# Optimization experiments

Measured on AMD Instinct MI355X. Metric: run time of the kernel, lower is better.

Reference implementation:

```python
import jax, jax.numpy as jnp
import numpy as np

EMB = 64
NUM_LAYERS = 2


def _mlp_embed(x, shift, scale, w1, b1, w2, b2):
    # PreNormLayer: (x + shift) * scale, then Linear-ReLU-Linear-ReLU
    x = (x + shift) * scale
    x = jax.nn.relu(x @ w1 + b1)
    return jax.nn.relu(x @ w2 + b2)


def _sage_conv(x_src, x_dst, src_idx, dst_idx, ll_w, ll_b, lr_w):
    # PyG SAGEConv: mean-aggregate gathered source features at destinations,
    # out = lin_l(mean) + lin_r(x_dst); lin_l has bias, lin_r does not.
    n_dst = x_dst.shape[0]
    msgs = x_src[src_idx]                                   # [E, D] gather
    ssum = jax.ops.segment_sum(msgs, dst_idx, num_segments=n_dst)
    cnt = jax.ops.segment_sum(jnp.ones(src_idx.shape[0], x_src.dtype),
                              dst_idx, num_segments=n_dst)
    mean = ssum / jnp.maximum(cnt, 1.0)[:, None]            # [n_dst, D]
    return mean @ ll_w + ll_b + x_dst @ lr_w


def setup_inputs() -> dict:
    key = jax.random.key(0)
    ks = jax.random.split(key, 20)
    n_cons, n_var, n_edges = 100_000, 200_000, 2_000_000
    cons_nf, var_nf, edge_nf = 5, 19, 1

    def lin(k, fan_in, fan_out):
        return jax.random.normal(k, (fan_in, fan_out), jnp.float32) / np.sqrt(fan_in)

    inp = {
        'cons_x': jax.random.normal(ks[0], (n_cons, cons_nf), jnp.float32),
        'var_x': jax.random.normal(ks[1], (n_var, var_nf), jnp.float32),
        'edge_attr': jax.random.normal(ks[2], (n_edges, edge_nf), jnp.float32),
        'edge_index': jnp.stack([
            jax.random.randint(ks[3], (n_edges,), 0, n_cons),
            jax.random.randint(ks[4], (n_edges,), 0, n_var)]).astype(jnp.int64),
        # constraint embedding MLP
        'cons_shift': 0.1 * jax.random.normal(ks[5], (cons_nf,), jnp.float32),
        'cons_scale': 1.0 + 0.1 * jax.random.normal(ks[6], (cons_nf,), jnp.float32),
        'cons_w1': lin(ks[7], cons_nf, EMB),
        'cons_b1': jnp.zeros((EMB,), jnp.float32),
        'cons_w2': lin(ks[8], EMB, EMB),
        'cons_b2': jnp.zeros((EMB,), jnp.float32),
        # variable embedding MLP
        'var_shift': 0.1 * jax.random.normal(ks[9], (var_nf,), jnp.float32),
        'var_scale': 1.0 + 0.1 * jax.random.normal(ks[10], (var_nf,), jnp.float32),
        'var_w1': lin(ks[11], var_nf, EMB),
        'var_b1': jnp.zeros((EMB,), jnp.float32),
        'var_w2': lin(ks[12], EMB, EMB),
        'var_b2': jnp.zeros((EMB,), jnp.float32),
        # edge PreNorm (computed but unused for conv_type='sage', as in source)
        'edge_shift': 0.1 * jax.random.normal(ks[13], (edge_nf,), jnp.float32),
        'edge_scale': 1.0 + 0.1 * jax.random.normal(ks[14], (edge_nf,), jnp.float32),
        # SAGEConv weights: [layer, direction(0: cons->var, 1: var->cons), in, out]
        'conv_ll_w': jax.random.normal(ks[15], (NUM_LAYERS, 2, EMB, EMB), jnp.float32) / np.sqrt(EMB),
        'conv_ll_b': jnp.zeros((NUM_LAYERS, 2, EMB), jnp.float32),
        'conv_lr_w': jax.random.normal(ks[16], (NUM_LAYERS, 2, EMB, EMB), jnp.float32) / np.sqrt(EMB),
    }
    return inp


def reference(cons_x, var_x, edge_attr, edge_index,
              cons_shift, cons_scale, cons_w1, cons_b1, cons_w2, cons_b2,
              var_shift, var_scale, var_w1, var_b1, var_w2, var_b2,
              edge_shift, edge_scale, conv_ll_w, conv_ll_b, conv_lr_w):
    x_c = _mlp_embed(cons_x, cons_shift, cons_scale, cons_w1, cons_b1, cons_w2, cons_b2)
    x_v = _mlp_embed(var_x, var_shift, var_scale, var_w1, var_b1, var_w2, var_b2)
    edge_feat = (edge_attr + edge_shift) * edge_scale  # unused for SAGE (faithful to source)
    del edge_feat
    src, dst = edge_index[0], edge_index[1]  # constraint -> variable
    for l in range(NUM_LAYERS):
        new_v = _sage_conv(x_c, x_v, src, dst, conv_ll_w[l, 0], conv_ll_b[l, 0], conv_lr_w[l, 0])
        new_c = _sage_conv(x_v, x_c, dst, src, conv_ll_w[l, 1], conv_ll_b[l, 1], conv_lr_w[l, 1])
        x_c, x_v = jax.nn.relu(new_c), jax.nn.relu(new_v)
    return x_v
```

## Files before the change

### kernel.cpp

```cpp
#include <hip/hip_runtime.h>

#define EMB 64
#define CH 4096


static __device__ __forceinline__ unsigned short f2bf(float x) {
    union { float f; unsigned u; } v; v.f = x;
    unsigned r = v.u + 0x7fffu + ((v.u >> 16) & 1u);
    return (unsigned short)(r >> 16);
}
static __device__ __forceinline__ float bflo(unsigned w) {
    union { unsigned u; float f; } v; v.u = w << 16; return v.f;
}
static __device__ __forceinline__ float bfhi(unsigned w) {
    union { unsigned u; float f; } v; v.u = w & 0xffff0000u; return v.f;
}

__global__ __launch_bounds__(256) void zero_int_kernel(int* __restrict__ p, int n) {
    int i = blockIdx.x * 256 + threadIdx.x;
    if (i < n) p[i] = 0;
}

__global__ __launch_bounds__(256) void scan_buckets_kernel(
    int* __restrict__ bc, int nbc, int* __restrict__ bv, int nbv, int E)
{
    __shared__ int sc[256];
    int t = threadIdx.x;
    {
        int v0 = (2 * t < nbc) ? bc[2 * t] : 0;
        int v1 = (2 * t + 1 < nbc) ? bc[2 * t + 1] : 0;
        sc[t] = v0 + v1;
        __syncthreads();
        for (int off = 1; off < 256; off <<= 1) {
            int x = (t >= off) ? sc[t - off] : 0;
            __syncthreads();
            sc[t] += x;
            __syncthreads();
        }
        int ex = (t > 0) ? sc[t - 1] : 0;
        if (2 * t < nbc) bc[2 * t] = ex;
        if (2 * t + 1 < nbc) bc[2 * t + 1] = ex + v0;
        if (t == 0) bc[nbc] = E;
        __syncthreads();
    }
    {
        int v0 = (2 * t < nbv) ? bv[2 * t] : 0;
        int v1 = (2 * t + 1 < nbv) ? bv[2 * t + 1] : 0;
        sc[t] = v0 + v1;
        __syncthreads();
        for (int off = 1; off < 256; off <<= 1) {
            int x = (t >= off) ? sc[t - off] : 0;
            __syncthreads();
            sc[t] += x;
            __syncthreads();
        }
        int ex = (t > 0) ? sc[t - 1] : 0;
        if (2 * t < nbv) bv[2 * t] = ex;
        if (2 * t + 1 < nbv) bv[2 * t + 1] = ex + v0;
        if (t == 0) bv[nbv] = E;
    }
}

__global__ __launch_bounds__(256) void bin_edges_kernel(
    const int* __restrict__ src, const int* __restrict__ dst, int E,
    int* __restrict__ gcur_c, int* __restrict__ gcur_v,
    unsigned* __restrict__ tmp_c, unsigned* __restrict__ tmp_v,
    int shc, int shv, int NBC, int NBV, int SLOTC, int SLOTV)
{
    __shared__ int hc[512], hv[512];
    int t = threadIdx.x;
    int base = blockIdx.x * CH;
    int n = min(CH, E - base);
    unsigned mc = (1u << shc) - 1u, mv = (1u << shv) - 1u;

    for (int i = t; i < NBC; i += 256) hc[i] = 0;
    for (int i = t; i < NBV; i += 256) hv[i] = 0;
    __syncthreads();

    int ss[16], dd[16];
#pragma unroll
    for (int q = 0; q < 16; ++q) {
        int li = t + q * 256;
        bool ok = li < n;
        ss[q] = ok ? src[base + li] : -1;
        dd[q] = ok ? dst[base + li] : -1;
        if (ok) {
            atomicAdd(&hc[ss[q] >> shc], 1);
            atomicAdd(&hv[dd[q] >> shv], 1);
        }
    }
    __syncthreads();

    for (int i = t; i < NBC; i += 256) {
        int c = hc[i];
        hc[i] = c ? (i * SLOTC + atomicAdd(&gcur_c[i], c)) : 0;
    }
    for (int i = t; i < NBV; i += 256) {
        int c = hv[i];
        hv[i] = c ? (i * SLOTV + atomicAdd(&gcur_v[i], c)) : 0;
    }
    __syncthreads();

#pragma unroll
    for (int q = 0; q < 16; ++q) {
        int li = t + q * 256;
        if (li < n) {
            unsigned s = (unsigned)ss[q], d = (unsigned)dd[q];
            int pc = atomicAdd(&hc[s >> shc], 1);
            tmp_c[pc] = ((s & mc) << 23) | d;
            int pv = atomicAdd(&hv[d >> shv], 1);
            tmp_v[pv] = ((d & mv) << 23) | s;
        }
    }
}

__global__ __launch_bounds__(256) void regroup2_dual_kernel(
    const unsigned* __restrict__ tmpA, const int* __restrict__ bbA,
    int* __restrict__ rpA, int* __restrict__ adjA, int nAn, int shA, int nbA, int slotA,
    const unsigned* __restrict__ tmpB, const int* __restrict__ bbB,
    int* __restrict__ rpB, int* __restrict__ adjB, int nBn, int shB, int nbB, int slotB, int E)
{
    __shared__ int cnt[512];
    __shared__ int offs[512];
    __shared__ int sc[256];
    const unsigned* tmp; const int* bb; int* rp; int* adj; int n_nodes, sh, nb, b, slot;
    if ((int)blockIdx.x < nbA) {
        tmp = tmpA; bb = bbA; rp = rpA; adj = adjA; n_nodes = nAn; sh = shA; nb = nbA; slot = slotA; b = blockIdx.x;
    } else {
        tmp = tmpB; bb = bbB; rp = rpB; adj = adjB; n_nodes = nBn; sh = shB; nb = nbB; slot = slotB; b = blockIdx.x - nbA;
    }
    int t = threadIdx.x;
    int node0 = b << sh;
    int node1 = min(node0 + (1 << sh), n_nodes);
    int nn = node1 - node0;
    for (int i = t; i < nn; i += 256) cnt[i] = 0;
    __syncthreads();
    int adjbase = bb[b];
    int cntb = bb[b + 1] - adjbase;
    int sbeg = b * slot;
    for (int e = sbeg + t; e < sbeg + cntb; e += 256)
        atomicAdd(&cnt[tmp[e] >> 23], 1);
    __syncthreads();
    int v0 = (2 * t < nn) ? cnt[2 * t] : 0;
    int v1 = (2 * t + 1 < nn) ? cnt[2 * t + 1] : 0;
    sc[t] = v0 + v1;
    __syncthreads();
    for (int off = 1; off < 256; off <<= 1) {
        int x = (t >= off) ? sc[t - off] : 0;
        __syncthreads();
        sc[t] += x;
        __syncthreads();
    }
    int ex = (t > 0) ? sc[t - 1] : 0;
    if (2 * t < nn) offs[2 * t] = ex;
    if (2 * t + 1 < nn) offs[2 * t + 1] = ex + v0;
    __syncthreads();
    for (int i = t; i < nn; i += 256) {
        rp[node0 + i] = adjbase + offs[i];
        cnt[i] = 0;
    }
    if (b == nb - 1 && t == 0) rp[n_nodes] = E;
    __syncthreads();
    for (int e = sbeg + t; e < sbeg + cntb; e += 256) {
        unsigned p = tmp[e];
        int d = (int)(p >> 23);
        int r = atomicAdd(&cnt[d], 1);
        adj[adjbase + offs[d] + r] = (int)(p & 0x7fffffu);
    }
}

template <int NF>
__device__ __forceinline__ void embed_body(
    float4* hsf, float* un,
    const float* __restrict__ x, const float* __restrict__ shift, const float* __restrict__ scale,
    const float* __restrict__ w1, const float* __restrict__ b1,
    const float* __restrict__ w2, const float* __restrict__ b2,
    const float* __restrict__ wll, const float* __restrict__ wlr,
    unsigned short* __restrict__ tb, float* __restrict__ u, int n, int bid)
{
    int t = threadIdx.x;
    long row0 = (long)bid * 64;
    int nrow = (n - row0 < 64) ? (int)(n - row0) : 64;

    float* xs  = un;
    float* w1s = un + NF * 68;

    for (int i = t; i < NF * EMB; i += 256) w1s[i] = w1[i];
    for (int i = t; i < 64 * NF; i += 256) {
        int r = i / NF, k = i - r * NF;
        float v = (r < nrow) ? x[row0 * NF + i] : 0.f;
        xs[k * 68 + r] = (v + shift[k]) * scale[k];
    }
    int rb = t >> 4;
    int r0 = rb * 4;
    int c0 = (t & 15) * 4;
    float4 b1v = *(const float4*)&b1[c0];
    float4 b2v = *(const float4*)&b2[c0];
    __syncthreads();

    float a[4][4];
#pragma unroll
    for (int i = 0; i < 4; ++i)
#pragma unroll
        for (int j = 0; j < 4; ++j) a[i][j] = 0.f;
#pragma unroll
    for (int k = 0; k < NF; ++k) {
        float4 xv = *(const float4*)&xs[k * 68 + r0];
        float4 wv = *(const float4*)&w1s[k * EMB + c0];
        float xa[4] = {xv.x, xv.y, xv.z, xv.w};
        float wa[4] = {wv.x, wv.y, wv.z, wv.w};
#pragma unroll
        for (int i = 0; i < 4; ++i)
#pragma unroll
            for (int j = 0; j < 4; ++j)
                a[i][j] = fmaf(xa[i], wa[j], a[i][j]);
    }
    __syncthreads();
    {
        float ba[4] = {b1v.x, b1v.y, b1v.z, b1v.w};
#pragma unroll
        for (int j = 0; j < 4; ++j) {
            int c = c0 + j;
            float4 o;
            o.x = fmaxf(a[0][j] + ba[j], 0.f);
            o.y = fmaxf(a[1][j] + ba[j], 0.f);
            o.z = fmaxf(a[2][j] + ba[j], 0.f);
            o.w = fmaxf(a[3][j] + ba[j], 0.f);
            hsf[c * 16 + (rb ^ (c & 15))] = o;
        }
    }
    {
        const float4* wg = (const float4*)w2;
        float4* wl = (float4*)un;
#pragma unroll
        for (int q = 0; q < 4; ++q) wl[t + q * 256] = wg[t + q * 256];
    }
    __syncthreads();

#pragma unroll
    for (int i = 0; i < 4; ++i)
#pragma unroll
        for (int j = 0; j < 4; ++j) a[i][j] = 0.f;
#pragma unroll 8
    for (int k = 0; k < EMB; ++k) {
        float4 xv = hsf[k * 16 + (rb ^ (k & 15))];
        float4 wv = *(const float4*)&un[k * EMB + c0];
        float xa[4] = {xv.x, xv.y, xv.z, xv.w};
        float wa[4] = {wv.x, wv.y, wv.z, wv.w};
#pragma unroll
        for (int i = 0; i < 4; ++i)
#pragma unroll
            for (int j = 0; j < 4; ++j)
                a[i][j] = fmaf(xa[i], wa[j], a[i][j]);
    }
    __syncthreads();
    {
        float ba[4] = {b2v.x, b2v.y, b2v.z, b2v.w};
#pragma unroll
        for (int j = 0; j < 4; ++j) {
            int c = c0 + j;
            float4 o;
            o.x = fmaxf(a[0][j] + ba[j], 0.f);
            o.y = fmaxf(a[1][j] + ba[j], 0.f);
            o.z = fmaxf(a[2][j] + ba[j], 0.f);
            o.w = fmaxf(a[3][j] + ba[j], 0.f);
            hsf[c * 16 + (rb ^ (c & 15))] = o;
        }
    }
    {
        const float4* wg = (const float4*)wll;
        float4* wl = (float4*)un;
#pragma unroll
        for (int q = 0; q < 4; ++q) wl[t + q * 256] = wg[t + q * 256];
    }
    __syncthreads();

#pragma unroll
    for (int i = 0; i < 4; ++i)
#pragma unroll
        for (int j = 0; j < 4; ++j) a[i][j] = 0.f;
#pragma unroll 8
    for (int k = 0; k < EMB; ++k) {
        float4 xv = hsf[k * 16 + (rb ^ (k & 15))];
        float4 wv = *(const float4*)&un[k * EMB + c0];
        float xa[4] = {xv.x, xv.y, xv.z, xv.w};
        float wa[4] = {wv.x, wv.y, wv.z, wv.w};
#pragma unroll
        for (int i = 0; i < 4; ++i)
#pragma unroll
            for (int j = 0; j < 4; ++j)
                a[i][j] = fmaf(xa[i], wa[j], a[i][j]);
    }
    __syncthreads();
    {
        const float4* wg = (const float4*)wlr;
        float4* wl = (float4*)un;
#pragma unroll
        for (int q = 0; q < 4; ++q) wl[t + q * 256] = wg[t + q * 256];
    }
#pragma unroll
    for (int i = 0; i < 4; ++i) {
        long gr = row0 + r0 + i;
        if (gr < n) {
            ushort4 o;
            o.x = f2bf(a[i][0]); o.y = f2bf(a[i][1]);
            o.z = f2bf(a[i][2]); o.w = f2bf(a[i][3]);
            *(ushort4*)(tb + gr * EMB + c0) = o;
        }
    }
    __syncthreads();

#pragma unroll
    for (int i = 0; i < 4; ++i)
#pragma unroll
        for (int j = 0; j < 4; ++j) a[i][j] = 0.f;
#pragma unroll 8
    for (int k = 0; k < EMB; ++k) {
        float4 xv = hsf[k * 16 + (rb ^ (k & 15))];
        float4 wv = *(const float4*)&un[k * EMB + c0];
        float xa[4] = {xv.x, xv.y, xv.z, xv.w};
        float wa[4] = {wv.x, wv.y, wv.z, wv.w};
#pragma unroll
        for (int i = 0; i < 4; ++i)
#pragma unroll
            for (int j = 0; j < 4; ++j)
                a[i][j] = fmaf(xa[i], wa[j], a[i][j]);
    }
#pragma unroll
    for (int i = 0; i < 4; ++i) {
        long gr = row0 + r0 + i;
        if (gr < n)
            *(float4*)&u[gr * EMB + c0] = make_float4(a[i][0], a[i][1], a[i][2], a[i][3]);
    }
}

template <int NFA, int NFB>
__global__ __launch_bounds__(256) void embed_dual_kernel(
    const float* xA, const float* shA, const float* scA,
    const float* w1A, const float* b1A, const float* w2A, const float* b2A,
    const float* wllA, const float* wlrA, unsigned short* tbA, float* uA, int nA,
    const float* xB, const float* shB, const float* scB,
    const float* w1B, const float* b1B, const float* w2B, const float* b2B,
    const float* wllB, const float* wlrB, unsigned short* tbB, float* uB, int nB,
    int split)
{
    __shared__ float4 hsf[1024];
    __shared__ __align__(16) float un[4096];
    if ((int)blockIdx.x < split)
        embed_body<NFA>(hsf, un, xA, shA, scA, w1A, b1A, w2A, b2A, wllA, wlrA, tbA, uA, nA, blockIdx.x);
    else
        embed_body<NFB>(hsf, un, xB, shB, scB, w1B, b1B, w2B, b2B, wllB, wlrB, tbB, uB, nB, blockIdx.x - split);
}

__global__ __launch_bounds__(256) void gemm64_dual_kernel(
    const float* __restrict__ XA, int nA, const float* __restrict__ WA, unsigned short* __restrict__ CA,
    const float* __restrict__ XB, int nB, const float* __restrict__ WB, float* __restrict__ CB, int split)
{
    __shared__ __align__(16) float xs[EMB * 68];
    __shared__ __align__(16) float w1s[EMB * EMB];

    const float* X; const float* W; int n; int bid; bool bf;
    if ((int)blockIdx.x < split) { X = XA; W = WA; n = nA; bid = blockIdx.x; bf = true; }
    else { X = XB; W = WB; n = nB; bid = blockIdx.x - split; bf = false; }

    int t = threadIdx.x;
    {
        int r = t >> 2;
        int cs = (t & 3) * 16;
        long gr = (long)bid * 64 + r;
        float4 v[4];
        if (gr < n) {
            const float4* sp = (const float4*)(X + gr * EMB + cs);
#pragma unroll
            for (int q = 0; q < 4; ++q) v[q] = sp[q];
        } else {
            float4 z = make_float4(0.f, 0.f, 0.f, 0.f);
#pragma unroll
            for (int q = 0; q < 4; ++q) v[q] = z;
        }
#pragma unroll
        for (int q = 0; q < 4; ++q) {
            xs[(cs + q * 4 + 0) * 68 + r] = v[q].x;
            xs[(cs + q * 4 + 1) * 68 + r] = v[q].y;
            xs[(cs + q * 4 + 2) * 68 + r] = v[q].z;
            xs[(cs + q * 4 + 3) * 68 + r] = v[q].w;
        }
        const float4* wg = (const float4*)W;
        float4* wl = (float4*)w1s;
#pragma unroll
        for (int q = 0; q < 4; ++q) wl[t + q * 256] = wg[t + q * 256];
    }
    __syncthreads();

    int r0 = (t >> 4) * 4;
    int c0 = (t & 15) * 4;
    float acc[4][4] = {{0.f}};
#pragma unroll 8
    for (int k = 0; k < EMB; ++k) {
        float4 xv = *(const float4*)&xs[k * 68 + r0];
        float4 wv = *(const float4*)&w1s[k * EMB + c0];
        float xa[4] = {xv.x, xv.y, xv.z, xv.w};
        float wa[4] = {wv.x, wv.y, wv.z, wv.w};
#pragma unroll
        for (int i = 0; i < 4; ++i)
#pragma unroll
            for (int j = 0; j < 4; ++j)
                acc[i][j] = fmaf(xa[i], wa[j], acc[i][j]);
    }

#pragma unroll
    for (int i = 0; i < 4; ++i) {
        long gr = (long)bid * 64 + r0 + i;
        if (gr < n) {
            if (bf) {
                ushort4 o;
                o.x = f2bf(acc[i][0]); o.y = f2bf(acc[i][1]);
                o.z = f2bf(acc[i][2]); o.w = f2bf(acc[i][3]);
                *(ushort4*)(CA + gr * EMB + c0) = o;
            } else {
                *(float4*)(CB + gr * EMB + c0) =
                    make_float4(acc[i][0], acc[i][1], acc[i][2], acc[i][3]);
            }
        }
    }
}

__global__ __launch_bounds__(256) void agg_rmw_kernel(
    const unsigned short* __restrict__ tbl, const int* __restrict__ rowptr,
    const int* __restrict__ adj, const float* __restrict__ bias,
    float* __restrict__ out, int n_dst)
{
    int t = threadIdx.x;
    int node = blockIdx.x * 16 + (t >> 4);
    if (node >= n_dst) return;
    int sub = t & 15;
    int p = sub & 7;
    int g = sub >> 3;
    int beg = rowptr[node];
    int end = rowptr[node + 1];
    const uint4* tb = (const uint4*)tbl;
    float a0 = 0.f, a1 = 0.f, a2 = 0.f, a3 = 0.f;
    float a4 = 0.f, a5 = 0.f, a6 = 0.f, a7 = 0.f;
    int e = beg + g;
    for (; e + 2 < end; e += 4) {
        int r0 = adj[e];
        int r1 = adj[e + 2];
        uint4 w0 = tb[(long)r0 * 8 + p];
        uint4 w1 = tb[(long)r1 * 8 + p];
        a0 += bflo(w0.x) + bflo(w1.x);
        a1 += bfhi(w0.x) + bfhi(w1.x);
        a2 += bflo(w0.y) + bflo(w1.y);
        a3 += bfhi(w0.y) + bfhi(w1.y);
        a4 += bflo(w0.z) + bflo(w1.z);
        a5 += bfhi(w0.z) + bfhi(w1.z);
        a6 += bflo(w0.w) + bflo(w1.w);
        a7 += bfhi(w0.w) + bfhi(w1.w);
    }
    if (e < end) {
        uint4 w0 = tb[(long)adj[e] * 8 + p];
        a0 += bflo(w0.x); a1 += bfhi(w0.x);
        a2 += bflo(w0.y); a3 += bfhi(w0.y);
        a4 += bflo(w0.z); a5 += bfhi(w0.z);
        a6 += bflo(w0.w); a7 += bfhi(w0.w);
    }
    a0 += __shfl_xor(a0, 8);
    a1 += __shfl_xor(a1, 8);
    a2 += __shfl_xor(a2, 8);
    a3 += __shfl_xor(a3, 8);
    a4 += __shfl_xor(a4, 8);
    a5 += __shfl_xor(a5, 8);
    a6 += __shfl_xor(a6, 8);
    a7 += __shfl_xor(a7, 8);
    if (g == 0) {
        int cnt = end - beg;
        float inv = 1.f / (float)(cnt > 0 ? cnt : 1);
        const float4* bp = (const float4*)bias + 2 * p;
        float4 bv0 = bp[0], bv1 = bp[1];
        float4* op = (float4*)(out + (long)node * EMB) + 2 * p;
        float4 ov0 = op[0], ov1 = op[1];
        float4 o0, o1;
        o0.x = fmaxf(a0 * inv + bv0.x + ov0.x, 0.f);
        o0.y = fmaxf(a1 * inv + bv0.y + ov0.y, 0.f);
        o0.z = fmaxf(a2 * inv + bv0.z + ov0.z, 0.f);
        o0.w = fmaxf(a3 * inv + bv0.w + ov0.w, 0.f);
        o1.x = fmaxf(a4 * inv + bv1.x + ov1.x, 0.f);
        o1.y = fmaxf(a5 * inv + bv1.y + ov1.y, 0.f);
        o1.z = fmaxf(a6 * inv + bv1.z + ov1.z, 0.f);
        o1.w = fmaxf(a7 * inv + bv1.w + ov1.w, 0.f);
        op[0] = o0;
        op[1] = o1;
    }
}

extern "C" void kernel_launch(void* const* d_in, const int* in_sizes, int n_in,
                              void* d_out, int out_size, void* d_ws, size_t ws_size,
                              hipStream_t stream) {
    const float* cons_x     = (const float*)d_in[0];
    const float* var_x      = (const float*)d_in[1];
    const int*   eidx       = (const int*)d_in[3];
    const float* cons_shift = (const float*)d_in[4];
    const float* cons_scale = (const float*)d_in[5];
    const float* cons_w1    = (const float*)d_in[6];
    const float* cons_b1    = (const float*)d_in[7];
    const float* cons_w2    = (const float*)d_in[8];
    const float* cons_b2    = (const float*)d_in[9];
    const float* var_shift  = (const float*)d_in[10];
    const float* var_scale  = (const float*)d_in[11];
    const float* var_w1     = (const float*)d_in[12];
    const float* var_b1     = (const float*)d_in[13];
    const float* var_w2     = (const float*)d_in[14];
    const float* var_b2     = (const float*)d_in[15];
    const float* ll_w       = (const float*)d_in[18];
    const float* ll_b       = (const float*)d_in[19];
    const float* lr_w       = (const float*)d_in[20];

    const int nC = in_sizes[0] / 5;
    const int nV = in_sizes[1] / 19;
    const int E  = in_sizes[3] / 2;
    const int* src = eidx;
    const int* dst = eidx + E;

    int shc = 0; while ((nC >> shc) >= 512) ++shc;
    int shv = 0; while ((nV >> shv) >= 512) ++shv;
    const int NBC = (nC + (1 << shc) - 1) >> shc;
    const int NBV = (nV + (1 << shv) - 1) >> shv;

    char* w = (char*)d_ws;
    auto alloc = [&](size_t bytes) {
        char* p = w;
        w += (bytes + 255) & ~(size_t)255;
        return p;
    };
    float* x_c = (float*)alloc((size_t)nC * EMB * 4);
    float* x_v = (float*)alloc((size_t)nV * EMB * 4);
    float* t_c = (float*)alloc((size_t)nC * EMB * 4);
    float* t_v = (float*)alloc((size_t)nV * EMB * 4);
    unsigned* tmp_c = (unsigned*)t_c;
    unsigned* tmp_v = (unsigned*)t_v;
    unsigned short* tb_c = (unsigned short*)t_c;
    unsigned short* tb_v = (unsigned short*)t_v;
    int* rp_v  = (int*)alloc((size_t)(nV + 1) * 4);
    int* rp_c  = (int*)alloc((size_t)(nC + 1) * 4);
    int* adj_v = (int*)alloc((size_t)E * 4);
    int* adj_c = (int*)alloc((size_t)E * 4);
    int* bkt   = (int*)alloc(2048 * 4);
    int* gcur_c = bkt;
    int* gcur_v = bkt + 1024;

    auto slot_for = [&](int NB, size_t cap_ints) {
        long s = 2L * E / NB;
        s = (s + 255) & ~255L;
        if (s < 4096) s = 4096;
        long cap = (long)(cap_ints / NB) & ~255L;
        if (s > cap) s = cap;
        return (int)s;
    };
    const int SLOTC = slot_for(NBC, (size_t)nC * EMB);
    const int SLOTV = slot_for(NBV, (size_t)nV * EMB);

    auto llw = [&](int l, int d) { return ll_w + (size_t)(l * 2 + d) * EMB * EMB; };
    auto lrw = [&](int l, int d) { return lr_w + (size_t)(l * 2 + d) * EMB * EMB; };
    auto llb = [&](int l, int d) { return ll_b + (size_t)(l * 2 + d) * EMB; };

    zero_int_kernel<<<8, 256, 0, stream>>>(bkt, 2048);
    bin_edges_kernel<<<(E + CH - 1) / CH, 256, 0, stream>>>(src, dst, E, gcur_c, gcur_v,
                                                            tmp_c, tmp_v, shc, shv, NBC, NBV,
                                                            SLOTC, SLOTV);
    scan_buckets_kernel<<<1, 256, 0, stream>>>(gcur_c, NBC, gcur_v, NBV, E);
    regroup2_dual_kernel<<<NBV + NBC, 256, 0, stream>>>(
        tmp_v, gcur_v, rp_v, adj_v, nV, shv, NBV, SLOTV,
        tmp_c, gcur_c, rp_c, adj_c, nC, shc, NBC, SLOTC, E);

    int gc = (nC + 63) / 64, gv = (nV + 63) / 64;
    embed_dual_kernel<5, 19><<<gc + gv, 256, 0, stream>>>(
        cons_x, cons_shift, cons_scale, cons_w1, cons_b1, cons_w2, cons_b2,
        llw(0, 0), lrw(0, 1), tb_c, x_c, nC,
        var_x, var_shift, var_scale, var_w1, var_b1, var_w2, var_b2,
        llw(0, 1), lrw(0, 0), tb_v, x_v, nV,
        gc);

    int gv16 = (nV + 15) / 16, gc16 = (nC + 15) / 16;
    agg_rmw_kernel<<<gv16, 256, 0, stream>>>(tb_c, rp_v, adj_v, llb(0, 0), x_v, nV);
    agg_rmw_kernel<<<gc16, 256, 0, stream>>>(tb_v, rp_c, adj_c, llb(0, 1), x_c, nC);

    gemm64_dual_kernel<<<gc + gv, 256, 0, stream>>>(
        x_c, nC, llw(1, 0), tb_c,
        x_v, nV, lrw(1, 0), (float*)d_out, gc);

    agg_rmw_kernel<<<gv16, 256, 0, stream>>>(tb_c, rp_v, adj_v, llb(1, 0), (float*)d_out, nV);
}
```

Baseline: 388.4 us.

## Read GEMM weights from global/L1 and shrink shared memory in embed/gemm kernels

Stops staging the weight matrices into shared memory in the embedding and dual-GEMM kernels and reads them straight from global memory, where they should stay L1/L2 resident. The activation tile moves to a padded stride-17 float4 layout, which replaces the XOR swizzle, and several barriers are dropped. This cuts LDS usage to raise occupancy and removes the weight-copy and sync overhead, at the cost of per-iteration global loads in the inner loops.

```diff
diff --git a/kernel.cpp b/kernel.cpp
--- a/kernel.cpp
+++ b/kernel.cpp
@@ -171,7 +171,7 @@
 
 template <int NF>
 __device__ __forceinline__ void embed_body(
-    float4* hsf, float* un,
+    float* xs, float4* hs,
     const float* __restrict__ x, const float* __restrict__ shift, const float* __restrict__ scale,
     const float* __restrict__ w1, const float* __restrict__ b1,
     const float* __restrict__ w2, const float* __restrict__ b2,
@@ -182,14 +182,10 @@
     long row0 = (long)bid * 64;
     int nrow = (n - row0 < 64) ? (int)(n - row0) : 64;
 
-    float* xs  = un;
-    float* w1s = un + NF * 68;
-
-    for (int i = t; i < NF * EMB; i += 256) w1s[i] = w1[i];
     for (int i = t; i < 64 * NF; i += 256) {
         int r = i / NF, k = i - r * NF;
         float v = (r < nrow) ? x[row0 * NF + i] : 0.f;
-        xs[k * 68 + r] = (v + shift[k]) * scale[k];
+        xs[i] = (v + shift[k]) * scale[k];
     }
     int rb = t >> 4;
     int r0 = rb * 4;
@@ -205,35 +201,31 @@
         for (int j = 0; j < 4; ++j) a[i][j] = 0.f;
 #pragma unroll
     for (int k = 0; k < NF; ++k) {
-        float4 xv = *(const float4*)&xs[k * 68 + r0];
-        float4 wv = *(const float4*)&w1s[k * EMB + c0];
-        float xa[4] = {xv.x, xv.y, xv.z, xv.w};
+        float x0 = xs[(r0 + 0) * NF + k];
+        float x1 = xs[(r0 + 1) * NF + k];
+        float x2 = xs[(r0 + 2) * NF + k];
+        float x3 = xs[(r0 + 3) * NF + k];
+        float4 wv = *(const float4*)&w1[k * EMB + c0];
         float wa[4] = {wv.x, wv.y, wv.z, wv.w};
 #pragma unroll
-        for (int i = 0; i < 4; ++i)
-#pragma unroll
-            for (int j = 0; j < 4; ++j)
-                a[i][j] = fmaf(xa[i], wa[j], a[i][j]);
-    }
-    __syncthreads();
+        for (int j = 0; j < 4; ++j) {
+            a[0][j] = fmaf(x0, wa[j], a[0][j]);
+            a[1][j] = fmaf(x1, wa[j], a[1][j]);
+            a[2][j] = fmaf(x2, wa[j], a[2][j]);
+            a[3][j] = fmaf(x3, wa[j], a[3][j]);
+        }
+    }
     {
         float ba[4] = {b1v.x, b1v.y, b1v.z, b1v.w};
 #pragma unroll
         for (int j = 0; j < 4; ++j) {
-            int c = c0 + j;
             float4 o;
             o.x = fmaxf(a[0][j] + ba[j], 0.f);
             o.y = fmaxf(a[1][j] + ba[j], 0.f);
             o.z = fmaxf(a[2][j] + ba[j], 0.f);
             o.w = fmaxf(a[3][j] + ba[j], 0.f);
-            hsf[c * 16 + (rb ^ (c & 15))] = o;
-        }
-    }
-    {
-        const float4* wg = (const float4*)w2;
-        float4* wl = (float4*)un;
-#pragma unroll
-        for (int q = 0; q < 4; ++q) wl[t + q * 256] = wg[t + q * 256];
+            hs[(c0 + j) * 17 + rb] = o;
+        }
     }
     __syncthreads();
 
@@ -243,8 +235,8 @@
         for (int j = 0; j < 4; ++j) a[i][j] = 0.f;
 #pragma unroll 8
     for (int k = 0; k < EMB; ++k) {
-        float4 xv = hsf[k * 16 + (rb ^ (k & 15))];
-        float4 wv = *(const float4*)&un[k * EMB + c0];
+        float4 xv = hs[k * 17 + rb];
+        float4 wv = *(const float4*)&w2[k * EMB + c0];
         float xa[4] = {xv.x, xv.y, xv.z, xv.w};
         float wa[4] = {wv.x, wv.y, wv.z, wv.w};
 #pragma unroll
@@ -258,20 +250,13 @@
         float ba[4] = {b2v.x, b2v.y, b2v.z, b2v.w};
 #pragma unroll
         for (int j = 0; j < 4; ++j) {
-            int c = c0 + j;
             float4 o;
             o.x = fmaxf(a[0][j] + ba[j], 0.f);
             o.y = fmaxf(a[1][j] + ba[j], 0.f);
             o.z = fmaxf(a[2][j] + ba[j], 0.f);
             o.w = fmaxf(a[3][j] + ba[j], 0.f);
-            hsf[c * 16 + (rb ^ (c & 15))] = o;
-        }
-    }
-    {
-        const float4* wg = (const float4*)wll;
-        float4* wl = (float4*)un;
-#pragma unroll
-        for (int q = 0; q < 4; ++q) wl[t + q * 256] = wg[t + q * 256];
+            hs[(c0 + j) * 17 + rb] = o;
+        }
     }
     __syncthreads();
 
@@ -281,8 +266,8 @@
         for (int j = 0; j < 4; ++j) a[i][j] = 0.f;
 #pragma unroll 8
     for (int k = 0; k < EMB; ++k) {
-        float4 xv = hsf[k * 16 + (rb ^ (k & 15))];
-        float4 wv = *(const float4*)&un[k * EMB + c0];
+        float4 xv = hs[k * 17 + rb];
+        float4 wv = *(const float4*)&wll[k * EMB + c0];
         float xa[4] = {xv.x, xv.y, xv.z, xv.w};
         float wa[4] = {wv.x, wv.y, wv.z, wv.w};
 #pragma unroll
@@ -290,13 +275,6 @@
 #pragma unroll
             for (int j = 0; j < 4; ++j)
                 a[i][j] = fmaf(xa[i], wa[j], a[i][j]);
-    }
-    __syncthreads();
-    {
-        const float4* wg = (const float4*)wlr;
-        float4* wl = (float4*)un;
-#pragma unroll
-        for (int q = 0; q < 4; ++q) wl[t + q * 256] = wg[t + q * 256];
     }
 #pragma unroll
     for (int i = 0; i < 4; ++i) {
@@ -308,7 +286,6 @@
             *(ushort4*)(tb + gr * EMB + c0) = o;
         }
     }
-    __syncthreads();
 
 #pragma unroll
     for (int i = 0; i < 4; ++i)
@@ -316,8 +293,8 @@
         for (int j = 0; j < 4; ++j) a[i][j] = 0.f;
 #pragma unroll 8
     for (int k = 0; k < EMB; ++k) {
-        float4 xv = hsf[k * 16 + (rb ^ (k & 15))];
-        float4 wv = *(const float4*)&un[k * EMB + c0];
+        float4 xv = hs[k * 17 + rb];
+        float4 wv = *(const float4*)&wlr[k * EMB + c0];
         float xa[4] = {xv.x, xv.y, xv.z, xv.w};
         float wa[4] = {wv.x, wv.y, wv.z, wv.w};
 #pragma unroll
@@ -344,20 +321,19 @@
     const float* wllB, const float* wlrB, unsigned short* tbB, float* uB, int nB,
     int split)
 {
-    __shared__ float4 hsf[1024];
-    __shared__ __align__(16) float un[4096];
+    __shared__ __align__(16) float xs[64 * (NFA > NFB ? NFA : NFB)];
+    __shared__ float4 hs[64 * 17];
     if ((int)blockIdx.x < split)
-        embed_body<NFA>(hsf, un, xA, shA, scA, w1A, b1A, w2A, b2A, wllA, wlrA, tbA, uA, nA, blockIdx.x);
+        embed_body<NFA>(xs, hs, xA, shA, scA, w1A, b1A, w2A, b2A, wllA, wlrA, tbA, uA, nA, blockIdx.x);
     else
-        embed_body<NFB>(hsf, un, xB, shB, scB, w1B, b1B, w2B, b2B, wllB, wlrB, tbB, uB, nB, blockIdx.x - split);
+        embed_body<NFB>(xs, hs, xB, shB, scB, w1B, b1B, w2B, b2B, wllB, wlrB, tbB, uB, nB, blockIdx.x - split);
 }
 
 __global__ __launch_bounds__(256) void gemm64_dual_kernel(
     const float* __restrict__ XA, int nA, const float* __restrict__ WA, unsigned short* __restrict__ CA,
     const float* __restrict__ XB, int nB, const float* __restrict__ WB, float* __restrict__ CB, int split)
 {
-    __shared__ __align__(16) float xs[EMB * 68];
-    __shared__ __align__(16) float w1s[EMB * EMB];
+    __shared__ float4 hs[64 * 17];
 
     const float* X; const float* W; int n; int bid; bool bf;
     if ((int)blockIdx.x < split) { X = XA; W = WA; n = nA; bid = blockIdx.x; bf = true; }
@@ -366,39 +342,29 @@
     int t = threadIdx.x;
     {
         int r = t >> 2;
-        int cs = (t & 3) * 16;
+        int q4 = (t & 3) * 4;
         long gr = (long)bid * 64 + r;
-        float4 v[4];
-        if (gr < n) {
-            const float4* sp = (const float4*)(X + gr * EMB + cs);
-#pragma unroll
-            for (int q = 0; q < 4; ++q) v[q] = sp[q];
-        } else {
-            float4 z = make_float4(0.f, 0.f, 0.f, 0.f);
-#pragma unroll
-            for (int q = 0; q < 4; ++q) v[q] = z;
-        }
+        const float4* sp = (const float4*)(X + gr * EMB) + (t & 3) * 4;
 #pragma unroll
         for (int q = 0; q < 4; ++q) {
-            xs[(cs + q * 4 + 0) * 68 + r] = v[q].x;
-            xs[(cs + q * 4 + 1) * 68 + r] = v[q].y;
-            xs[(cs + q * 4 + 2) * 68 + r] = v[q].z;
-            xs[(cs + q * 4 + 3) * 68 + r] = v[q].w;
-        }
-        const float4* wg = (const float4*)W;
-        float4* wl = (float4*)w1s;
-#pragma unroll
-        for (int q = 0; q < 4; ++q) wl[t + q * 256] = wg[t + q * 256];
-    }
-    __syncthreads();
-
-    int r0 = (t >> 4) * 4;
+            float4 v = (gr < n) ? sp[q] : make_float4(0.f, 0.f, 0.f, 0.f);
+            int c = q4 * 4 + q * 4;
+            ((float*)&hs[(c + 0) * 17])[r] = v.x;
+            ((float*)&hs[(c + 1) * 17])[r] = v.y;
+            ((float*)&hs[(c + 2) * 17])[r] = v.z;
+            ((float*)&hs[(c + 3) * 17])[r] = v.w;
+        }
+    }
+    __syncthreads();
+
+    int rb = t >> 4;
+    int r0 = rb * 4;
     int c0 = (t & 15) * 4;
     float acc[4][4] = {{0.f}};
 #pragma unroll 8
     for (int k = 0; k < EMB; ++k) {
-        float4 xv = *(const float4*)&xs[k * 68 + r0];
-        float4 wv = *(const float4*)&w1s[k * EMB + c0];
+        float4 xv = hs[k * 17 + rb];
+        float4 wv = *(const float4*)&W[k * EMB + c0];
         float xa[4] = {xv.x, xv.y, xv.z, xv.w};
         float wa[4] = {wv.x, wv.y, wv.z, wv.w};
 #pragma unroll
```

Result: slower. 410.7 us (+5.7%).
